# Optimization experiments

Measured on AMD Instinct MI355X. Metric: run time of the kernel, lower is better.

The kernel has to match this reference:

```python
import jax, jax.numpy as jnp
import numpy as np

B, SQ, SK, D, H = 2, 2048, 2048, 1024, 16
DK = D // H


def setup_inputs() -> dict:
    key = jax.random.key(0)
    ks = jax.random.split(key, 16)
    s = 1.0 / np.sqrt(D)
    inp = {
        "query": jax.random.normal(ks[0], (B, SQ, D), jnp.float32),
        "key": jax.random.normal(ks[1], (B, SK, D), jnp.float32),
        "value": jax.random.normal(ks[2], (B, SK, D), jnp.float32),
        "R": jax.random.normal(ks[3], (B, SK, D), jnp.float32),
        "Wq": jax.random.normal(ks[4], (D, D), jnp.float32) * s,
        "bq": jnp.zeros((D,), jnp.float32),
        "Wv": jax.random.normal(ks[5], (D, D), jnp.float32) * s,
        "bv": jnp.zeros((D,), jnp.float32),
        "Wr": jax.random.normal(ks[6], (D, D), jnp.float32) * s,
        "br": jnp.zeros((D,), jnp.float32),
        "W_h": jax.random.normal(ks[7], (H, DK, DK), jnp.float32) * (1.0 / np.sqrt(DK)),
        "Wo": jax.random.normal(ks[8], (D, D), jnp.float32) * s,
        "bo": jnp.zeros((D,), jnp.float32),
    }
    return inp


def _forward(query, key, value, R, Wq, bq, Wv, bv, Wr, br, W_h, Wo, bo):
    scale = 1.0 / np.sqrt(DK)
    # projections (torch Linear: x @ W.T + b)
    Q = (query @ Wq.T + bq).reshape(B, SQ, H, DK).transpose(0, 2, 1, 3)   # (B,H,SQ,DK)
    V = (value @ Wv.T + bv).reshape(B, SK, H, DK).transpose(0, 2, 1, 3)   # (B,H,SK,DK)
    Rp = (R @ Wr.T + br).reshape(B, SK, H, DK).transpose(0, 2, 1, 3)      # (B,H,SK,DK)
    # torch einsum 'hnk,bhn->bhn' sums W_h over its last axis -> elementwise gate
    w_rowsum = W_h.sum(axis=-1)  # (H, DK)

    def step(h, r_t):
        h_new = jnp.tanh(h * w_rowsum + r_t)  # (B,H,DK)
        return h_new, h_new

    h0 = jnp.zeros((B, H, DK), Rp.dtype)
    Rt = Rp.transpose(2, 0, 1, 3)  # (SK,B,H,DK)
    _, Hs = jax.lax.scan(step, h0, Rt)
    Hst = Hs.transpose(1, 2, 0, 3)  # (B,H,SK,DK)

    scores = jnp.einsum('bhqd,bhkd->bhqk', Q, Hst) * scale
    attn = jax.nn.softmax(scores, axis=-1)
    out = jnp.einsum('bhqk,bhkd->bhqd', attn, V)
    out = out.transpose(0, 2, 1, 3).reshape(B, SQ, D)
    return out @ Wo.T + bo


def reference(query, key, value, R, Wq, bq, Wv, bv, Wr, br, W_h, Wo, bo):
    return _forward(query, key, value, R, Wq, bq, Wv, bv, Wr, br, W_h, Wo, bo)
```

## Files before the change

kernel.cpp:

```cpp
#include <hip/hip_runtime.h>
#include <stdint.h>

typedef unsigned short u16;
typedef __attribute__((ext_vector_type(8))) _Float16 h8;
typedef __attribute__((ext_vector_type(2))) __fp16 hp2;
typedef __attribute__((ext_vector_type(4))) float f4;

#define B_ 2
#define SQ_ 2048
#define SK_ 2048
#define D_ 1024
#define H_ 16
#define DK_ 64

__device__ __forceinline__ u16 f2h(float f) {
  union { _Float16 h; u16 u; } v; v.h = (_Float16)f; return v.u;
}
__device__ __forceinline__ float h2f(u16 b) {
  union { u16 u; _Float16 h; } v; v.u = b; return (float)v.h;
}
__device__ __forceinline__ unsigned pkrtz(float a, float b) {
  union { hp2 h; unsigned u; } v; v.h = __builtin_amdgcn_cvt_pkrtz(a, b); return v.u;
}
__device__ __forceinline__ float fexp2(float x) {
  float r;
  asm("v_exp_f32 %0, %1" : "=v"(r) : "v"(x));
  return r;
}

typedef const void __attribute__((address_space(1)))* gas1;
typedef void __attribute__((address_space(3)))* las3;
__device__ __forceinline__ void gld16(const void* g, void* l) {
  __builtin_amdgcn_global_load_lds((gas1)g, (las3)l, 16, 0, 0);
}

__global__ void rma_cast(const float* __restrict__ xq, const float* __restrict__ xv,
                         const float* __restrict__ xr, const float* __restrict__ w0,
                         const float* __restrict__ w1, const float* __restrict__ w2,
                         const float* __restrict__ w3, u16* __restrict__ oq,
                         u16* __restrict__ ov, u16* __restrict__ orr,
                         u16* __restrict__ o0, u16* __restrict__ o1,
                         u16* __restrict__ o2, u16* __restrict__ o3) {
  const int z = blockIdx.z;
  if (z >= 3 && blockIdx.x >= 512) return;
  const float* src;
  u16* dst;
  switch (z) {
    case 0: src = xq; dst = oq; break;
    case 1: src = xv; dst = ov; break;
    case 2: src = xr; dst = orr; break;
    case 3: src = w0; dst = o0; break;
    case 4: src = w1; dst = o1; break;
    case 5: src = w2; dst = o2; break;
    default: src = w3; dst = o3; break;
  }
  int i = (blockIdx.x * 256 + threadIdx.x) * 8;
  float4 a = *(const float4*)(src + i);
  float4 b = *(const float4*)(src + i + 4);
  alignas(16) u16 t[8] = {f2h(a.x), f2h(a.y), f2h(a.z), f2h(a.w),
                          f2h(b.x), f2h(b.y), f2h(b.z), f2h(b.w)};
  *(int4*)(dst + i) = *(int4*)t;
}

__device__ __forceinline__ void gemm_mainloop(
    const u16* __restrict__ A, const u16* __restrict__ Bw, int K,
    u16* As, u16* Bs, int m0, int n0, f4 (&acc)[4][4]) {
  const int tid = threadIdx.x;
  const int w = tid >> 6, lane = tid & 63;
  const int quad = lane >> 4, ln = lane & 15;
  const int wm = (w >> 1) * 64, wn = (w & 1) * 64;
  const int c0 = tid, c1 = tid + 256;
  const u16* a0 = A + (size_t)(m0 + (c0 >> 2)) * K + (c0 & 3) * 8;
  const u16* a1 = A + (size_t)(m0 + (c1 >> 2)) * K + (c1 & 3) * 8;
  const u16* b0 = Bw + (size_t)(n0 + (c0 >> 2)) * K + (c0 & 3) * 8;
  const u16* b1 = Bw + (size_t)(n0 + (c1 >> 2)) * K + (c1 & 3) * 8;
  u16* As0 = As + (0 + w * 64) * 8;
  u16* As1 = As + (256 + w * 64) * 8;
  u16* Bs0 = Bs + (0 + w * 64) * 8;
  u16* Bs1 = Bs + (256 + w * 64) * 8;
  for (int kt = 0; kt < K; kt += 32) {
    gld16(a0 + kt, As0);
    gld16(a1 + kt, As1);
    gld16(b0 + kt, Bs0);
    gld16(b1 + kt, Bs1);
    __syncthreads();
    h8 af[4], bf[4];
#pragma unroll
    for (int i = 0; i < 4; i++)
      af[i] = *(const h8*)&As[(wm + i * 16 + ln) * 32 + quad * 8];
#pragma unroll
    for (int i = 0; i < 4; i++)
      bf[i] = *(const h8*)&Bs[(wn + i * 16 + ln) * 32 + quad * 8];
#pragma unroll
    for (int i = 0; i < 4; i++)
#pragma unroll
      for (int j = 0; j < 4; j++)
        acc[i][j] = __builtin_amdgcn_mfma_f32_16x16x32_f16(af[i], bf[j], acc[i][j], 0, 0, 0);
    __syncthreads();
  }
}

__device__ __forceinline__ void gemm_mainloop64(
    const u16* __restrict__ A, const u16* __restrict__ Bw, int K,
    u16* As, u16* Bs, int m0, int n0, f4 (&acc)[2][4]) {
  const int tid = threadIdx.x;
  const int w = tid >> 6, lane = tid & 63;
  const int quad = lane >> 4, ln = lane & 15;
  const int wm = (w >> 1) * 32, wn = (w & 1) * 64;
  const u16* a0 = A + (size_t)(m0 + (tid >> 2)) * K + (tid & 3) * 8;
  const u16* b0 = Bw + (size_t)(n0 + (tid >> 2)) * K + (tid & 3) * 8;
  const u16* b1 = Bw + (size_t)(n0 + ((tid + 256) >> 2)) * K + (tid & 3) * 8;
  u16* As0 = As + (w * 64) * 8;
  u16* Bs0 = Bs + (w * 64) * 8;
  u16* Bs1 = Bs + (256 + w * 64) * 8;
  for (int kt = 0; kt < K; kt += 32) {
    gld16(a0 + kt, As0);
    gld16(b0 + kt, Bs0);
    gld16(b1 + kt, Bs1);
    __syncthreads();
    h8 af[2], bf[4];
#pragma unroll
    for (int i = 0; i < 2; i++)
      af[i] = *(const h8*)&As[(wm + i * 16 + ln) * 32 + quad * 8];
#pragma unroll
    for (int j = 0; j < 4; j++)
      bf[j] = *(const h8*)&Bs[(wn + j * 16 + ln) * 32 + quad * 8];
#pragma unroll
    for (int i = 0; i < 2; i++)
#pragma unroll
      for (int j = 0; j < 4; j++)
        acc[i][j] = __builtin_amdgcn_mfma_f32_16x16x32_f16(af[i], bf[j], acc[i][j], 0, 0, 0);
    __syncthreads();
  }
}

__global__ __launch_bounds__(256, 2)
void rma_proj_gemm(const u16* __restrict__ Xq, const u16* __restrict__ Xv,
                   const u16* __restrict__ Xr, const u16* __restrict__ Wq,
                   const u16* __restrict__ Wv, const u16* __restrict__ Wr,
                   const float* __restrict__ bq, const float* __restrict__ bv,
                   const float* __restrict__ br, u16* __restrict__ Qb,
                   u16* __restrict__ Vt, float* __restrict__ Rp) {
  const int z = blockIdx.z;
  const u16* A = z == 0 ? Xq : (z == 1 ? Xv : Xr);
  const u16* Bw = z == 0 ? Wq : (z == 1 ? Wv : Wr);
  const float* bias = z == 0 ? bq : (z == 1 ? bv : br);
  __shared__ u16 As[128 * 32];
  __shared__ u16 Bs[128 * 32];
  const int m0 = blockIdx.x * 128, n0 = blockIdx.y * 128;
  f4 acc[4][4] = {};
  gemm_mainloop(A, Bw, D_, As, Bs, m0, n0, acc);
  const int tid = threadIdx.x;
  const int w = tid >> 6, lane = tid & 63;
  const int quad = lane >> 4, ln = lane & 15;
  const int wm = (w >> 1) * 64, wn = (w & 1) * 64;
#pragma unroll
  for (int i = 0; i < 4; i++)
#pragma unroll
    for (int j = 0; j < 4; j++) {
      const int colg = n0 + wn + j * 16 + ln;
      const float bb = bias[colg];
      const int h = colg >> 6, d = colg & 63;
      const int row4 = m0 + wm + i * 16 + quad * 4;
      const int b = row4 >> 11, s = row4 & 2047;
      if (z == 1) {
        uint2 pk;
        pk.x = pkrtz(acc[i][j][0] + bb, acc[i][j][1] + bb);
        pk.y = pkrtz(acc[i][j][2] + bb, acc[i][j][3] + bb);
        *(uint2*)&Vt[((size_t)((b * H_ + h) * DK_ + d)) * SK_ + s] = pk;
      } else {
#pragma unroll
        for (int r = 0; r < 4; r++) {
          const float v = acc[i][j][r] + bb;
          const size_t idx = ((size_t)(b * H_ + h) * SK_ + (s + r)) * DK_ + d;
          if (z == 2) Rp[idx] = v;
          else Qb[idx] = f2h(v);
        }
      }
    }
}

__global__ __launch_bounds__(256, 2)
void rma_final_gemm(const u16* __restrict__ Og, const u16* __restrict__ Wo,
                    const float* __restrict__ bo, float* __restrict__ out) {
  __shared__ u16 As[64 * 32];
  __shared__ u16 Bs[128 * 32];
  const int m0 = blockIdx.x * 64, n0 = blockIdx.y * 128;
  f4 acc[2][4] = {};
  gemm_mainloop64(Og, Wo, D_, As, Bs, m0, n0, acc);
  const int tid = threadIdx.x;
  const int w = tid >> 6, lane = tid & 63;
  const int quad = lane >> 4, ln = lane & 15;
  const int wm = (w >> 1) * 32, wn = (w & 1) * 64;
#pragma unroll
  for (int i = 0; i < 2; i++)
#pragma unroll
    for (int j = 0; j < 4; j++) {
      const int colg = n0 + wn + j * 16 + ln;
      const float bb = bo[colg];
#pragma unroll
      for (int r = 0; r < 4; r++) {
        const int rowg = m0 + wm + i * 16 + quad * 4 + r;
        out[(size_t)rowg * D_ + colg] = acc[i][j][r] + bb;
      }
    }
}

#define RB_ 32
__global__ __launch_bounds__(64)
void rma_recurrence(const float* __restrict__ Rp, const float* __restrict__ Wh,
                    u16* __restrict__ Hst) {
  const int bh = blockIdx.x;
  const int d = threadIdx.x;
  const int h = bh & 15;
  const float* wr = Wh + (h * 64 + d) * 64;
  float ws = 0.f;
#pragma unroll
  for (int k = 0; k < 64; k += 4) {
    float4 wv = *(const float4*)(wr + k);
    ws += (wv.x + wv.y) + (wv.z + wv.w);
  }
  const float C2 = 2.885390081777927f;
  const float wc = ws * C2;
  const size_t base = (size_t)bh * (SK_ * DK_) + d;
  const float* r = Rp + base;
  u16* o = Hst + base;
  float cur[RB_], nxt[RB_];
#pragma unroll
  for (int j = 0; j < RB_; j++) cur[j] = r[(size_t)j * DK_];
  float hs = 0.f;
  for (int t0 = 0; t0 < SK_; t0 += RB_) {
    const int tn = (t0 + RB_ < SK_) ? (t0 + RB_) : t0;
#pragma unroll
    for (int j = 0; j < RB_; j++) nxt[j] = r[(size_t)(tn + j) * DK_];
#pragma unroll
    for (int j = 0; j < RB_; j++) {
      const float cc = cur[j] * C2;
      float x = __builtin_fmaf(hs, wc, cc);
      float e = fexp2(x);
      float inv = __builtin_amdgcn_rcpf(e + 1.0f);
      hs = __builtin_fmaf(-2.0f, inv, 1.0f);
      o[(size_t)(t0 + j) * DK_] = f2h(hs);
    }
#pragma unroll
    for (int j = 0; j < RB_; j++) cur[j] = nxt[j];
  }
}

#define FXM_ 12.0f
__global__ __launch_bounds__(256, 2)
void rma_flash(const u16* __restrict__ Qb, const u16* __restrict__ Hst,
               const u16* __restrict__ Vt, u16* __restrict__ Og) {
  __shared__ u16 Kt[64 * 72];
  __shared__ u16 Vts[64 * 72];
  __shared__ u16 Ps[4][32 * 72];
  const int tid = threadIdx.x;
  const int w = tid >> 6, lane = tid & 63;
  const int quad = lane >> 4, ln = lane & 15;
  const int bh = blockIdx.y;
  const int q0 = blockIdx.x * 128 + w * 32;
  const float scale2 = 0.18033688011112042f;
  const u16* Qg = Qb + (size_t)bh * SQ_ * DK_;
  const u16* Kg = Hst + (size_t)bh * SK_ * DK_;
  const u16* Vg = Vt + (size_t)bh * DK_ * SK_;
  u16* Pw = Ps[w];
  h8 qf[2][2];
#pragma unroll
  for (int qt = 0; qt < 2; qt++)
#pragma unroll
    for (int c = 0; c < 2; c++)
      qf[qt][c] = *(const h8*)&Qg[(size_t)(q0 + qt * 16 + ln) * DK_ + c * 32 + quad * 8];
  f4 o[4][2] = {};
  float l[2] = {0.f, 0.f};

  const int c0 = tid, c1 = tid + 256;
  const int r0 = c0 >> 3, o0 = (c0 & 7) * 8;
  const int r1 = c1 >> 3, o1 = (c1 & 7) * 8;
  const u16* kg0 = Kg + (size_t)r0 * DK_ + o0;
  const u16* kg1 = Kg + (size_t)r1 * DK_ + o1;
  const u16* vg0 = Vg + (size_t)r0 * SK_ + o0;
  const u16* vg1 = Vg + (size_t)r1 * SK_ + o1;
  u16* kl0 = &Kt[r0 * 72 + o0];
  u16* kl1 = &Kt[r1 * 72 + o1];
  u16* vl0 = &Vts[r0 * 72 + o0];
  u16* vl1 = &Vts[r1 * 72 + o1];

  int4 ks0 = *(const int4*)(kg0);
  int4 ks1 = *(const int4*)(kg1);
  int4 vs0 = *(const int4*)(vg0);
  int4 vs1 = *(const int4*)(vg1);

  for (int kt = 0; kt < SK_; kt += 64) {
    __syncthreads();
    *(int4*)kl0 = ks0;
    *(int4*)kl1 = ks1;
    *(int4*)vl0 = vs0;
    *(int4*)vl1 = vs1;
    __syncthreads();
    h8 kf[4][2], vf[4][2];
#pragma unroll
    for (int m = 0; m < 4; m++) {
      kf[m][0] = *(const h8*)&Kt[(m * 16 + ln) * 72 + quad * 8];
      kf[m][1] = *(const h8*)&Kt[(m * 16 + ln) * 72 + 32 + quad * 8];
    }
#pragma unroll
    for (int dt = 0; dt < 4; dt++) {
      vf[dt][0] = *(const h8*)&Vts[(dt * 16 + ln) * 72 + quad * 8];
      vf[dt][1] = *(const h8*)&Vts[(dt * 16 + ln) * 72 + 32 + quad * 8];
    }
    const int ktn = (kt + 64 < SK_) ? kt + 64 : 0;
    ks0 = *(const int4*)(kg0 + (size_t)ktn * DK_);
    ks1 = *(const int4*)(kg1 + (size_t)ktn * DK_);
    vs0 = *(const int4*)(vg0 + ktn);
    vs1 = *(const int4*)(vg1 + ktn);
    f4 st[4][2];
#pragma unroll
    for (int m = 0; m < 4; m++)
#pragma unroll
      for (int qt = 0; qt < 2; qt++) {
        f4 t = {0.f, 0.f, 0.f, 0.f};
        t = __builtin_amdgcn_mfma_f32_16x16x32_f16(kf[m][0], qf[qt][0], t, 0, 0, 0);
        t = __builtin_amdgcn_mfma_f32_16x16x32_f16(kf[m][1], qf[qt][1], t, 0, 0, 0);
        st[m][qt] = t;
      }
#pragma unroll
    for (int qt = 0; qt < 2; qt++)
#pragma unroll
      for (int m = 0; m < 4; m++) {
        const float p0 = fexp2(__builtin_fmaf(st[m][qt][0], scale2, -FXM_));
        const float p1 = fexp2(__builtin_fmaf(st[m][qt][1], scale2, -FXM_));
        const float p2 = fexp2(__builtin_fmaf(st[m][qt][2], scale2, -FXM_));
        const float p3 = fexp2(__builtin_fmaf(st[m][qt][3], scale2, -FXM_));
        l[qt] += (p0 + p1) + (p2 + p3);
        uint2 pk;
        pk.x = pkrtz(p0, p1);
        pk.y = pkrtz(p2, p3);
        *(uint2*)&Pw[(qt * 16 + ln) * 72 + m * 16 + quad * 4] = pk;
      }
    asm volatile("" ::: "memory");
#pragma unroll
    for (int c = 0; c < 2; c++) {
      h8 pb0 = *(const h8*)&Pw[(0 + ln) * 72 + c * 32 + quad * 8];
      h8 pb1 = *(const h8*)&Pw[(16 + ln) * 72 + c * 32 + quad * 8];
#pragma unroll
      for (int dt = 0; dt < 4; dt++) {
        o[dt][0] = __builtin_amdgcn_mfma_f32_16x16x32_f16(vf[dt][c], pb0, o[dt][0], 0, 0, 0);
        o[dt][1] = __builtin_amdgcn_mfma_f32_16x16x32_f16(vf[dt][c], pb1, o[dt][1], 0, 0, 0);
      }
    }
  }
  const int b = bh >> 4, h = bh & 15;
#pragma unroll
  for (int qt = 0; qt < 2; qt++) {
    float lq = l[qt];
    lq += __shfl_xor(lq, 16);
    lq += __shfl_xor(lq, 32);
    const float linv = __builtin_amdgcn_rcpf(lq);
    const int q = q0 + qt * 16 + ln;
#pragma unroll
    for (int dt = 0; dt < 4; dt++) {
      uint2 pk;
      pk.x = pkrtz(o[dt][qt][0] * linv, o[dt][qt][1] * linv);
      pk.y = pkrtz(o[dt][qt][2] * linv, o[dt][qt][3] * linv);
      *(uint2*)&Og[((size_t)b * SQ_ + q) * D_ + h * DK_ + dt * 16 + quad * 4] = pk;
    }
  }
}

extern "C" void kernel_launch(void* const* d_in, const int* in_sizes, int n_in,
                              void* d_out, int out_size, void* d_ws, size_t ws_size,
                              hipStream_t stream) {
  const float* query = (const float*)d_in[0];
  const float* value = (const float*)d_in[2];
  const float* R = (const float*)d_in[3];
  const float* Wq = (const float*)d_in[4];
  const float* bq = (const float*)d_in[5];
  const float* Wv = (const float*)d_in[6];
  const float* bv = (const float*)d_in[7];
  const float* Wr = (const float*)d_in[8];
  const float* br = (const float*)d_in[9];
  const float* W_h = (const float*)d_in[10];
  const float* Wo = (const float*)d_in[11];
  const float* bo = (const float*)d_in[12];
  float* out = (float*)d_out;

  char* ws = (char*)d_ws;
  const size_t MB = 1 << 20;
  u16* Xq = (u16*)(ws + 0 * MB);
  u16* Xv = (u16*)(ws + 8 * MB);
  u16* Xr = (u16*)(ws + 16 * MB);
  u16* Wqb = (u16*)(ws + 24 * MB);
  u16* Wvb = (u16*)(ws + 26 * MB);
  u16* Wrb = (u16*)(ws + 28 * MB);
  u16* Wob = (u16*)(ws + 30 * MB);
  u16* Qb = (u16*)(ws + 32 * MB);
  u16* Vt = (u16*)(ws + 40 * MB);
  float* Rp = (float*)(ws + 48 * MB);
  u16* Hs = (u16*)(ws + 64 * MB);
  u16* Og = (u16*)(ws + 72 * MB);

  rma_cast<<<dim3(2048, 1, 7), 256, 0, stream>>>(query, value, R, Wq, Wv, Wr, Wo,
                                                 Xq, Xv, Xr, Wqb, Wvb, Wrb, Wob);
  rma_proj_gemm<<<dim3(32, 8, 3), 256, 0, stream>>>(Xq, Xv, Xr, Wqb, Wvb, Wrb,
                                                    bq, bv, br, Qb, Vt, Rp);
  rma_recurrence<<<dim3(32), 64, 0, stream>>>(Rp, W_h, Hs);
  rma_flash<<<dim3(16, 32), 256, 0, stream>>>(Qb, Hs, Vt, Og);
  rma_final_gemm<<<dim3(64, 8), 256, 0, stream>>>(Og, Wob, bo, out);
}
```

Measured before the change: 302.3 us.

## Overlap serial recurrence with Q/V projections and casts with R projection

Restructures the pipeline so the R projection runs first. The remaining casts run as extra blocks in the same launch, and the latency-bound tanh recurrence shares a launch with the Q and V projection GEMMs at raised wave priority. The recurrence is also spread across 8 blocks of 256 threads instead of 32 blocks of 64. Its body is reordered so the next exponent depends on the reciprocal directly, which shortens the serial dependency chain. The aim is to hide the long sequential scan behind GEMM work. The cost is heterogeneous blocks and possible resource contention with the co-scheduled GEMM blocks.

```diff
diff --git a/kernel.cpp b/kernel.cpp
--- a/kernel.cpp
+++ b/kernel.cpp
@@ -34,32 +34,22 @@
   __builtin_amdgcn_global_load_lds((gas1)g, (las3)l, 16, 0, 0);
 }
 
-__global__ void rma_cast(const float* __restrict__ xq, const float* __restrict__ xv,
-                         const float* __restrict__ xr, const float* __restrict__ w0,
-                         const float* __restrict__ w1, const float* __restrict__ w2,
-                         const float* __restrict__ w3, u16* __restrict__ oq,
-                         u16* __restrict__ ov, u16* __restrict__ orr,
-                         u16* __restrict__ o0, u16* __restrict__ o1,
-                         u16* __restrict__ o2, u16* __restrict__ o3) {
-  const int z = blockIdx.z;
-  if (z >= 3 && blockIdx.x >= 512) return;
-  const float* src;
-  u16* dst;
-  switch (z) {
-    case 0: src = xq; dst = oq; break;
-    case 1: src = xv; dst = ov; break;
-    case 2: src = xr; dst = orr; break;
-    case 3: src = w0; dst = o0; break;
-    case 4: src = w1; dst = o1; break;
-    case 5: src = w2; dst = o2; break;
-    default: src = w3; dst = o3; break;
-  }
-  int i = (blockIdx.x * 256 + threadIdx.x) * 8;
+__device__ __forceinline__ void cast8(const float* __restrict__ src,
+                                      u16* __restrict__ dst, int i) {
   float4 a = *(const float4*)(src + i);
   float4 b = *(const float4*)(src + i + 4);
   alignas(16) u16 t[8] = {f2h(a.x), f2h(a.y), f2h(a.z), f2h(a.w),
                           f2h(b.x), f2h(b.y), f2h(b.z), f2h(b.w)};
   *(int4*)(dst + i) = *(int4*)t;
+}
+
+__global__ void rma_cast_rwr(const float* __restrict__ xr, const float* __restrict__ wr,
+                             u16* __restrict__ orr, u16* __restrict__ owr) {
+  const int b = blockIdx.x;
+  const float* src; u16* dst; int bi;
+  if (b < 2048) { src = xr; dst = orr; bi = b; }
+  else          { src = wr; dst = owr; bi = b - 2048; }
+  cast8(src, dst, (bi * 256 + threadIdx.x) * 8);
 }
 
 __device__ __forceinline__ void gemm_mainloop(
@@ -135,19 +125,110 @@
 }
 
 __global__ __launch_bounds__(256, 2)
-void rma_proj_gemm(const u16* __restrict__ Xq, const u16* __restrict__ Xv,
-                   const u16* __restrict__ Xr, const u16* __restrict__ Wq,
-                   const u16* __restrict__ Wv, const u16* __restrict__ Wr,
-                   const float* __restrict__ bq, const float* __restrict__ bv,
-                   const float* __restrict__ br, u16* __restrict__ Qb,
-                   u16* __restrict__ Vt, float* __restrict__ Rp) {
-  const int z = blockIdx.z;
-  const u16* A = z == 0 ? Xq : (z == 1 ? Xv : Xr);
-  const u16* Bw = z == 0 ? Wq : (z == 1 ? Wv : Wr);
-  const float* bias = z == 0 ? bq : (z == 1 ? bv : br);
+void rma_projr_cast(const u16* __restrict__ Xr, const u16* __restrict__ Wrb,
+                    const float* __restrict__ br, float* __restrict__ Rp,
+                    const float* __restrict__ xq, const float* __restrict__ xv,
+                    const float* __restrict__ wq, const float* __restrict__ wv,
+                    const float* __restrict__ wo, u16* __restrict__ oxq,
+                    u16* __restrict__ oxv, u16* __restrict__ owq,
+                    u16* __restrict__ owv, u16* __restrict__ owo) {
   __shared__ u16 As[128 * 32];
   __shared__ u16 Bs[128 * 32];
-  const int m0 = blockIdx.x * 128, n0 = blockIdx.y * 128;
+  const int b = blockIdx.x;
+  if (b >= 256) {
+    const int c = b - 256;
+    const float* src; u16* dst; int bi;
+    if (c < 2048)       { src = xq; dst = oxq; bi = c; }
+    else if (c < 4096)  { src = xv; dst = oxv; bi = c - 2048; }
+    else if (c < 4608)  { src = wq; dst = owq; bi = c - 4096; }
+    else if (c < 5120)  { src = wv; dst = owv; bi = c - 4608; }
+    else                { src = wo; dst = owo; bi = c - 5120; }
+    cast8(src, dst, (bi * 256 + threadIdx.x) * 8);
+    return;
+  }
+  const int m0 = (b & 31) * 128, n0 = (b >> 5) * 128;
+  f4 acc[4][4] = {};
+  gemm_mainloop(Xr, Wrb, D_, As, Bs, m0, n0, acc);
+  const int tid = threadIdx.x;
+  const int w = tid >> 6, lane = tid & 63;
+  const int quad = lane >> 4, ln = lane & 15;
+  const int wm = (w >> 1) * 64, wn = (w & 1) * 64;
+#pragma unroll
+  for (int i = 0; i < 4; i++)
+#pragma unroll
+    for (int j = 0; j < 4; j++) {
+      const int colg = n0 + wn + j * 16 + ln;
+      const float bb = br[colg];
+      const int h = colg >> 6, d = colg & 63;
+      const int row4 = m0 + wm + i * 16 + quad * 4;
+      const int bb_i = row4 >> 11, s = row4 & 2047;
+#pragma unroll
+      for (int r = 0; r < 4; r++) {
+        const size_t idx = ((size_t)(bb_i * H_ + h) * SK_ + (s + r)) * DK_ + d;
+        Rp[idx] = acc[i][j][r] + bb;
+      }
+    }
+}
+
+#define RB_ 32
+__global__ __launch_bounds__(256, 2)
+void rma_recur_projqv(const float* __restrict__ Rp, const float* __restrict__ Wh,
+                      u16* __restrict__ Hst, const u16* __restrict__ Xq,
+                      const u16* __restrict__ Xv, const u16* __restrict__ Wqb,
+                      const u16* __restrict__ Wvb, const float* __restrict__ bq,
+                      const float* __restrict__ bv, u16* __restrict__ Qb,
+                      u16* __restrict__ Vt) {
+  __shared__ u16 As[128 * 32];
+  __shared__ u16 Bs[128 * 32];
+  const int blk = blockIdx.x;
+  if (blk < 8) {
+    __builtin_amdgcn_s_setprio(2);
+    const int ch = blk * 256 + threadIdx.x;
+    const int bh = ch >> 6, d = ch & 63, h = bh & 15;
+    const float* wr = Wh + (h * 64 + d) * 64;
+    float ws = 0.f;
+#pragma unroll
+    for (int k = 0; k < 64; k += 4) {
+      float4 wv4 = *(const float4*)(wr + k);
+      ws += (wv4.x + wv4.y) + (wv4.z + wv4.w);
+    }
+    const float C2 = 2.885390081777927f;
+    const float wsC2 = ws * C2;
+    const float Kw = 2.0f * wsC2;
+    const size_t base = (size_t)bh * (SK_ * DK_) + d;
+    const float* r = Rp + base;
+    u16* o = Hst + base;
+    float cur[RB_], nxt[RB_];
+#pragma unroll
+    for (int j = 0; j < RB_; j++) cur[j] = r[(size_t)j * DK_];
+    float e = fexp2(cur[0] * C2);
+    for (int t0 = 0; t0 < SK_; t0 += RB_) {
+      const int tn = (t0 + RB_ < SK_) ? (t0 + RB_) : t0;
+#pragma unroll
+      for (int j = 0; j < RB_; j++) nxt[j] = r[(size_t)(tn + j) * DK_];
+#pragma unroll
+      for (int j = 0; j < RB_; j++) {
+        const float a = e + 1.0f;
+        const float bb = __builtin_amdgcn_rcpf(a);
+        const float hs = __builtin_fmaf(-2.0f, bb, 1.0f);
+        o[(size_t)(t0 + j) * DK_] = f2h(hs);
+        const float rn = (j + 1 < RB_) ? cur[j + 1] : nxt[0];
+        const float K = __builtin_fmaf(C2, rn, wsC2);
+        const float x = __builtin_fmaf(-Kw, bb, K);
+        e = fexp2(x);
+      }
+#pragma unroll
+      for (int j = 0; j < RB_; j++) cur[j] = nxt[j];
+    }
+    return;
+  }
+  const int pb = blk - 8;
+  const int z = pb >> 8;
+  const int t = pb & 255;
+  const int m0 = (t & 31) * 128, n0 = (t >> 5) * 128;
+  const u16* A = z == 0 ? Xq : Xv;
+  const u16* Bw = z == 0 ? Wqb : Wvb;
+  const float* bias = z == 0 ? bq : bv;
   f4 acc[4][4] = {};
   gemm_mainloop(A, Bw, D_, As, Bs, m0, n0, acc);
   const int tid = threadIdx.x;
@@ -173,8 +254,7 @@
         for (int r = 0; r < 4; r++) {
           const float v = acc[i][j][r] + bb;
           const size_t idx = ((size_t)(b * H_ + h) * SK_ + (s + r)) * DK_ + d;
-          if (z == 2) Rp[idx] = v;
-          else Qb[idx] = f2h(v);
+          Qb[idx] = f2h(v);
         }
       }
     }
@@ -204,47 +284,6 @@
         out[(size_t)rowg * D_ + colg] = acc[i][j][r] + bb;
       }
     }
-}
-
-#define RB_ 32
-__global__ __launch_bounds__(64)
-void rma_recurrence(const float* __restrict__ Rp, const float* __restrict__ Wh,
-                    u16* __restrict__ Hst) {
-  const int bh = blockIdx.x;
-  const int d = threadIdx.x;
-  const int h = bh & 15;
-  const float* wr = Wh + (h * 64 + d) * 64;
-  float ws = 0.f;
-#pragma unroll
-  for (int k = 0; k < 64; k += 4) {
-    float4 wv = *(const float4*)(wr + k);
-    ws += (wv.x + wv.y) + (wv.z + wv.w);
-  }
-  const float C2 = 2.885390081777927f;
-  const float wc = ws * C2;
-  const size_t base = (size_t)bh * (SK_ * DK_) + d;
-  const float* r = Rp + base;
-  u16* o = Hst + base;
-  float cur[RB_], nxt[RB_];
-#pragma unroll
-  for (int j = 0; j < RB_; j++) cur[j] = r[(size_t)j * DK_];
-  float hs = 0.f;
-  for (int t0 = 0; t0 < SK_; t0 += RB_) {
-    const int tn = (t0 + RB_ < SK_) ? (t0 + RB_) : t0;
-#pragma unroll
-    for (int j = 0; j < RB_; j++) nxt[j] = r[(size_t)(tn + j) * DK_];
-#pragma unroll
-    for (int j = 0; j < RB_; j++) {
-      const float cc = cur[j] * C2;
-      float x = __builtin_fmaf(hs, wc, cc);
-      float e = fexp2(x);
-      float inv = __builtin_amdgcn_rcpf(e + 1.0f);
-      hs = __builtin_fmaf(-2.0f, inv, 1.0f);
-      o[(size_t)(t0 + j) * DK_] = f2h(hs);
-    }
-#pragma unroll
-    for (int j = 0; j < RB_; j++) cur[j] = nxt[j];
-  }
 }
 
 #define FXM_ 12.0f
@@ -399,11 +438,12 @@
   u16* Hs = (u16*)(ws + 64 * MB);
   u16* Og = (u16*)(ws + 72 * MB);
 
-  rma_cast<<<dim3(2048, 1, 7), 256, 0, stream>>>(query, value, R, Wq, Wv, Wr, Wo,
-                                                 Xq, Xv, Xr, Wqb, Wvb, Wrb, Wob);
-  rma_proj_gemm<<<dim3(32, 8, 3), 256, 0, stream>>>(Xq, Xv, Xr, Wqb, Wvb, Wrb,
-                                                    bq, bv, br, Qb, Vt, Rp);
-  rma_recurrence<<<dim3(32), 64, 0, stream>>>(Rp, W_h, Hs);
+  rma_cast_rwr<<<dim3(2560), 256, 0, stream>>>(R, Wr, Xr, Wrb);
+  rma_projr_cast<<<dim3(5888), 256, 0, stream>>>(Xr, Wrb, br, Rp,
+                                                 query, value, Wq, Wv, Wo,
+                                                 Xq, Xv, Wqb, Wvb, Wob);
+  rma_recur_projqv<<<dim3(520), 256, 0, stream>>>(Rp, W_h, Hs, Xq, Xv, Wqb, Wvb,
+                                                  bq, bv, Qb, Vt);
   rma_flash<<<dim3(16, 32), 256, 0, stream>>>(Qb, Hs, Vt, Og);
   rma_final_gemm<<<dim3(64, 8), 256, 0, stream>>>(Og, Wob, bo, out);
 }
```

Result: faster. 293.7 us (-2.8%).

## Fuse recurrence and flash attention with progress flags to overlap them

Applied to the files above, without the earlier changes.

Merges the serial tanh recurrence and the flash attention into one persistent launch. The first 8 blocks run the recurrence and publish per-head progress counters with atomic release stores. The flash blocks spin-wait on those counters before consuming each chunk of keys, which hides the long serial recurrence behind attention work. The recurrence step is also reformulated to shorten the dependent chain, and the cast kernel is flattened to a 1D grid that also zeroes the control flags. The spin-wait has a timeout fallback, and the scheme relies on the recurrence blocks being scheduled before the flash blocks that wait on them, which risks wrong results or stalls.

```diff
diff --git a/kernel.cpp b/kernel.cpp
--- a/kernel.cpp
+++ b/kernel.cpp
@@ -13,11 +13,11 @@
 #define H_ 16
 #define DK_ 64
 
+#define C_PROG  0
+#define CTRL_N  512
+
 __device__ __forceinline__ u16 f2h(float f) {
   union { _Float16 h; u16 u; } v; v.h = (_Float16)f; return v.u;
-}
-__device__ __forceinline__ float h2f(u16 b) {
-  union { u16 u; _Float16 h; } v; v.u = b; return (float)v.h;
 }
 __device__ __forceinline__ unsigned pkrtz(float a, float b) {
   union { hp2 h; unsigned u; } v; v.h = __builtin_amdgcn_cvt_pkrtz(a, b); return v.u;
@@ -34,32 +34,47 @@
   __builtin_amdgcn_global_load_lds((gas1)g, (las3)l, 16, 0, 0);
 }
 
-__global__ void rma_cast(const float* __restrict__ xq, const float* __restrict__ xv,
-                         const float* __restrict__ xr, const float* __restrict__ w0,
-                         const float* __restrict__ w1, const float* __restrict__ w2,
-                         const float* __restrict__ w3, u16* __restrict__ oq,
-                         u16* __restrict__ ov, u16* __restrict__ orr,
-                         u16* __restrict__ o0, u16* __restrict__ o1,
-                         u16* __restrict__ o2, u16* __restrict__ o3) {
-  const int z = blockIdx.z;
-  if (z >= 3 && blockIdx.x >= 512) return;
-  const float* src;
-  u16* dst;
-  switch (z) {
-    case 0: src = xq; dst = oq; break;
-    case 1: src = xv; dst = ov; break;
-    case 2: src = xr; dst = orr; break;
-    case 3: src = w0; dst = o0; break;
-    case 4: src = w1; dst = o1; break;
-    case 5: src = w2; dst = o2; break;
-    default: src = w3; dst = o3; break;
-  }
-  int i = (blockIdx.x * 256 + threadIdx.x) * 8;
+__device__ __forceinline__ void spin_ge(int* p, int v) {
+  if (__hip_atomic_load(p, __ATOMIC_RELAXED, __HIP_MEMORY_SCOPE_AGENT) >= v) return;
+  int n = 0;
+  for (;;) {
+    __builtin_amdgcn_s_sleep(16);
+    int x = ((++n & 63) == 0)
+                ? __hip_atomic_load(p, __ATOMIC_ACQUIRE, __HIP_MEMORY_SCOPE_AGENT)
+                : __hip_atomic_load(p, __ATOMIC_RELAXED, __HIP_MEMORY_SCOPE_AGENT);
+    if (x >= v) return;
+    if (n > 8192) return;
+  }
+}
+
+__device__ __forceinline__ void cast8(const float* __restrict__ src,
+                                      u16* __restrict__ dst, int i) {
   float4 a = *(const float4*)(src + i);
   float4 b = *(const float4*)(src + i + 4);
   alignas(16) u16 t[8] = {f2h(a.x), f2h(a.y), f2h(a.z), f2h(a.w),
                           f2h(b.x), f2h(b.y), f2h(b.z), f2h(b.w)};
   *(int4*)(dst + i) = *(int4*)t;
+}
+
+__global__ void rma_cast_all(const float* __restrict__ xq, const float* __restrict__ xv,
+                             const float* __restrict__ xr, const float* __restrict__ wq,
+                             const float* __restrict__ wv, const float* __restrict__ wr,
+                             const float* __restrict__ wo, u16* __restrict__ oxq,
+                             u16* __restrict__ oxv, u16* __restrict__ oxr,
+                             u16* __restrict__ owq, u16* __restrict__ owv,
+                             u16* __restrict__ owr, u16* __restrict__ owo,
+                             int* __restrict__ ctrl) {
+  const int b = blockIdx.x;
+  if (b == 0) { ctrl[threadIdx.x] = 0; ctrl[256 + threadIdx.x] = 0; }
+  const float* src; u16* dst; int bi;
+  if (b < 2048)      { src = xq; dst = oxq; bi = b; }
+  else if (b < 4096) { src = xv; dst = oxv; bi = b - 2048; }
+  else if (b < 6144) { src = xr; dst = oxr; bi = b - 4096; }
+  else if (b < 6656) { src = wq; dst = owq; bi = b - 6144; }
+  else if (b < 7168) { src = wv; dst = owv; bi = b - 6656; }
+  else if (b < 7680) { src = wr; dst = owr; bi = b - 7168; }
+  else               { src = wo; dst = owo; bi = b - 7680; }
+  cast8(src, dst, (bi * 256 + threadIdx.x) * 8);
 }
 
 __device__ __forceinline__ void gemm_mainloop(
@@ -180,90 +195,74 @@
     }
 }
 
-__global__ __launch_bounds__(256, 2)
-void rma_final_gemm(const u16* __restrict__ Og, const u16* __restrict__ Wo,
-                    const float* __restrict__ bo, float* __restrict__ out) {
-  __shared__ u16 As[64 * 32];
-  __shared__ u16 Bs[128 * 32];
-  const int m0 = blockIdx.x * 64, n0 = blockIdx.y * 128;
-  f4 acc[2][4] = {};
-  gemm_mainloop64(Og, Wo, D_, As, Bs, m0, n0, acc);
-  const int tid = threadIdx.x;
-  const int w = tid >> 6, lane = tid & 63;
-  const int quad = lane >> 4, ln = lane & 15;
-  const int wm = (w >> 1) * 32, wn = (w & 1) * 64;
-#pragma unroll
-  for (int i = 0; i < 2; i++)
-#pragma unroll
-    for (int j = 0; j < 4; j++) {
-      const int colg = n0 + wn + j * 16 + ln;
-      const float bb = bo[colg];
-#pragma unroll
-      for (int r = 0; r < 4; r++) {
-        const int rowg = m0 + wm + i * 16 + quad * 4 + r;
-        out[(size_t)rowg * D_ + colg] = acc[i][j][r] + bb;
-      }
-    }
-}
-
 #define RB_ 32
-__global__ __launch_bounds__(64)
-void rma_recurrence(const float* __restrict__ Rp, const float* __restrict__ Wh,
-                    u16* __restrict__ Hst) {
-  const int bh = blockIdx.x;
-  const int d = threadIdx.x;
-  const int h = bh & 15;
+__device__ void recur_run(const float* __restrict__ Rp, const float* __restrict__ Wh,
+                          u16* __restrict__ Hst, int* ctrl) {
+  __builtin_amdgcn_s_setprio(2);
+  const int tid = threadIdx.x;
+  const int ch = blockIdx.x * 256 + tid;
+  const int bh = ch >> 6, d = ch & 63, h = bh & 15;
   const float* wr = Wh + (h * 64 + d) * 64;
   float ws = 0.f;
 #pragma unroll
   for (int k = 0; k < 64; k += 4) {
-    float4 wv = *(const float4*)(wr + k);
-    ws += (wv.x + wv.y) + (wv.z + wv.w);
+    float4 wv4 = *(const float4*)(wr + k);
+    ws += (wv4.x + wv4.y) + (wv4.z + wv4.w);
   }
   const float C2 = 2.885390081777927f;
-  const float wc = ws * C2;
+  const float wsC2 = ws * C2;
+  const float Kw = 2.0f * wsC2;
   const size_t base = (size_t)bh * (SK_ * DK_) + d;
   const float* r = Rp + base;
   u16* o = Hst + base;
+  int* pg = ctrl + C_PROG + bh * 16;
   float cur[RB_], nxt[RB_];
 #pragma unroll
   for (int j = 0; j < RB_; j++) cur[j] = r[(size_t)j * DK_];
-  float hs = 0.f;
+  float e = fexp2(cur[0] * C2);
   for (int t0 = 0; t0 < SK_; t0 += RB_) {
-    const int tn = (t0 + RB_ < SK_) ? (t0 + RB_) : t0;
+    const int t1 = t0 + RB_;
+    const int tn = (t1 < SK_) ? t1 : t0;
 #pragma unroll
     for (int j = 0; j < RB_; j++) nxt[j] = r[(size_t)(tn + j) * DK_];
 #pragma unroll
     for (int j = 0; j < RB_; j++) {
-      const float cc = cur[j] * C2;
-      float x = __builtin_fmaf(hs, wc, cc);
-      float e = fexp2(x);
-      float inv = __builtin_amdgcn_rcpf(e + 1.0f);
-      hs = __builtin_fmaf(-2.0f, inv, 1.0f);
+      const float a = e + 1.0f;
+      const float bb = __builtin_amdgcn_rcpf(a);
+      const float hs = __builtin_fmaf(-2.0f, bb, 1.0f);
       o[(size_t)(t0 + j) * DK_] = f2h(hs);
-    }
+      const float rn = (j + 1 < RB_) ? cur[j + 1] : nxt[0];
+      const float K = __builtin_fmaf(C2, rn, wsC2);
+      const float x = __builtin_fmaf(-Kw, bb, K);
+      e = fexp2(x);
+    }
+    if (((t1 & 127) == 0) && (tid & 63) == 0)
+      __hip_atomic_store(pg, t1, __ATOMIC_RELEASE, __HIP_MEMORY_SCOPE_AGENT);
 #pragma unroll
     for (int j = 0; j < RB_; j++) cur[j] = nxt[j];
   }
+  __builtin_amdgcn_s_setprio(0);
 }
 
 #define FXM_ 12.0f
-__global__ __launch_bounds__(256, 2)
-void rma_flash(const u16* __restrict__ Qb, const u16* __restrict__ Hst,
-               const u16* __restrict__ Vt, u16* __restrict__ Og) {
-  __shared__ u16 Kt[64 * 72];
-  __shared__ u16 Vts[64 * 72];
-  __shared__ u16 Ps[4][32 * 72];
+__device__ void flash_task(int fidx, const u16* __restrict__ Qb,
+                           const u16* __restrict__ Hst, const u16* __restrict__ Vt,
+                           u16* __restrict__ Og, u16* smem, int* ctrl) {
   const int tid = threadIdx.x;
   const int w = tid >> 6, lane = tid & 63;
   const int quad = lane >> 4, ln = lane & 15;
-  const int bh = blockIdx.y;
-  const int q0 = blockIdx.x * 128 + w * 32;
+  const int bh = fidx >> 4, qtile = fidx & 15;
+  const int q0 = qtile * 128 + w * 32;
+  u16* Kt = smem;
+  u16* Vts = smem + 64 * 72;
+  u16* Pw = smem + 2 * 64 * 72 + w * (32 * 72);
   const float scale2 = 0.18033688011112042f;
   const u16* Qg = Qb + (size_t)bh * SQ_ * DK_;
   const u16* Kg = Hst + (size_t)bh * SK_ * DK_;
   const u16* Vg = Vt + (size_t)bh * DK_ * SK_;
-  u16* Pw = Ps[w];
+  int* pg = ctrl + C_PROG + bh * 16;
+  if (tid == 0) spin_ge(pg, 128);
+  __syncthreads();
   h8 qf[2][2];
 #pragma unroll
   for (int qt = 0; qt < 2; qt++)
@@ -272,7 +271,6 @@
       qf[qt][c] = *(const h8*)&Qg[(size_t)(q0 + qt * 16 + ln) * DK_ + c * 32 + quad * 8];
   f4 o[4][2] = {};
   float l[2] = {0.f, 0.f};
-
   const int c0 = tid, c1 = tid + 256;
   const int r0 = c0 >> 3, o0 = (c0 & 7) * 8;
   const int r1 = c1 >> 3, o1 = (c1 & 7) * 8;
@@ -284,13 +282,16 @@
   u16* kl1 = &Kt[r1 * 72 + o1];
   u16* vl0 = &Vts[r0 * 72 + o0];
   u16* vl1 = &Vts[r1 * 72 + o1];
-
   int4 ks0 = *(const int4*)(kg0);
   int4 ks1 = *(const int4*)(kg1);
   int4 vs0 = *(const int4*)(vg0);
   int4 vs1 = *(const int4*)(vg1);
-
+  int seen = 128;
   for (int kt = 0; kt < SK_; kt += 64) {
+    if (tid == 0) {
+      const int need = (kt + 128 <= SK_) ? kt + 128 : SK_;
+      if (seen < need) { spin_ge(pg, need); seen = need; }
+    }
     __syncthreads();
     *(int4*)kl0 = ks0;
     *(int4*)kl1 = ks1;
@@ -365,6 +366,45 @@
       *(uint2*)&Og[((size_t)b * SQ_ + q) * D_ + h * DK_ + dt * 16 + quad * 4] = pk;
     }
   }
+}
+
+__global__ __launch_bounds__(256, 2)
+void rma_recur_flash(const float* __restrict__ Rp, const float* __restrict__ Wh,
+                     u16* __restrict__ Hst, const u16* __restrict__ Qb,
+                     const u16* __restrict__ Vt, u16* __restrict__ Og,
+                     int* __restrict__ ctrl) {
+  __shared__ __align__(16) u16 smem[18432];
+  if (blockIdx.x < 8) {
+    recur_run(Rp, Wh, Hst, ctrl);
+    return;
+  }
+  flash_task(blockIdx.x - 8, Qb, Hst, Vt, Og, smem, ctrl);
+}
+
+__global__ __launch_bounds__(256, 2)
+void rma_final_gemm(const u16* __restrict__ Og, const u16* __restrict__ Wo,
+                    const float* __restrict__ bo, float* __restrict__ out) {
+  __shared__ u16 As[64 * 32];
+  __shared__ u16 Bs[128 * 32];
+  const int m0 = blockIdx.x * 64, n0 = blockIdx.y * 128;
+  f4 acc[2][4] = {};
+  gemm_mainloop64(Og, Wo, D_, As, Bs, m0, n0, acc);
+  const int tid = threadIdx.x;
+  const int w = tid >> 6, lane = tid & 63;
+  const int quad = lane >> 4, ln = lane & 15;
+  const int wm = (w >> 1) * 32, wn = (w & 1) * 64;
+#pragma unroll
+  for (int i = 0; i < 2; i++)
+#pragma unroll
+    for (int j = 0; j < 4; j++) {
+      const int colg = n0 + wn + j * 16 + ln;
+      const float bb = bo[colg];
+#pragma unroll
+      for (int r = 0; r < 4; r++) {
+        const int rowg = m0 + wm + i * 16 + quad * 4 + r;
+        out[(size_t)rowg * D_ + colg] = acc[i][j][r] + bb;
+      }
+    }
 }
 
 extern "C" void kernel_launch(void* const* d_in, const int* in_sizes, int n_in,
@@ -398,12 +438,12 @@
   float* Rp = (float*)(ws + 48 * MB);
   u16* Hs = (u16*)(ws + 64 * MB);
   u16* Og = (u16*)(ws + 72 * MB);
-
-  rma_cast<<<dim3(2048, 1, 7), 256, 0, stream>>>(query, value, R, Wq, Wv, Wr, Wo,
-                                                 Xq, Xv, Xr, Wqb, Wvb, Wrb, Wob);
+  int* ctrl = (int*)(ws + 80 * MB);
+
+  rma_cast_all<<<dim3(8192), 256, 0, stream>>>(query, value, R, Wq, Wv, Wr, Wo,
+                                               Xq, Xv, Xr, Wqb, Wvb, Wrb, Wob, ctrl);
   rma_proj_gemm<<<dim3(32, 8, 3), 256, 0, stream>>>(Xq, Xv, Xr, Wqb, Wvb, Wrb,
                                                     bq, bv, br, Qb, Vt, Rp);
-  rma_recurrence<<<dim3(32), 64, 0, stream>>>(Rp, W_h, Hs);
-  rma_flash<<<dim3(16, 32), 256, 0, stream>>>(Qb, Hs, Vt, Og);
+  rma_recur_flash<<<dim3(520), 256, 0, stream>>>(Rp, W_h, Hs, Qb, Vt, Og, ctrl);
   rma_final_gemm<<<dim3(64, 8), 256, 0, stream>>>(Og, Wob, bo, out);
 }
```

Result: faster. 286.0 us (-5.4%).
